# Kernel optimization log

Hardware: AMD Instinct MI355X
Metric: run time of the kernel (lower is better)

The kernel has to match this reference:

```python
import jax, jax.numpy as jnp
import numpy as np

B, T, D, H, DK, DV, FF = 4, 1024, 1024, 16, 64, 64, 4096


def setup_inputs() -> dict:
    key = jax.random.key(0)
    ks = jax.random.split(key, 16)
    sc = 0.02  # init scale (original uses uninitialized torch.empty; use small randn)
    n = lambda k, shape: jax.random.normal(k, shape, jnp.float32) * sc
    return dict(
        x=jax.random.normal(ks[0], (B, T, D), jnp.float32),
        y=jax.random.normal(ks[1], (B, T, D), jnp.float32),
        Wq1=n(ks[2], (H, D, DK)), Wk1=n(ks[3], (H, D, DK)),
        Wv1=n(ks[4], (H, D, DV)), Wo1=n(ks[5], (D, D)),
        Wq2=n(ks[6], (H, D, DK)), Wk2=n(ks[7], (H, D, DK)),
        Wv2=n(ks[8], (H, D, DV)), Wo2=n(ks[9], (D, D)),
        W_in=n(ks[10], (FF, D)), b_in=jnp.zeros((FF,), jnp.float32),
        W_out=n(ks[11], (D, FF)), b_out=jnp.zeros((D,), jnp.float32),
    )


def _mha(q, k, v, Wq, Wk, Wv, Wo):
    # per-head projections: (B,T,D) x (H,D,dk) -> (B,H,T,dk)
    WQ = jnp.einsum('btd,hdk->bhtk', q, Wq)
    WK = jnp.einsum('bsd,hdk->bhsk', k, Wk)
    WV = jnp.einsum('bsd,hdv->bhsv', v, Wv)
    scores = jnp.einsum('bhtk,bhsk->bhts', WQ, WK) / jnp.sqrt(jnp.float32(DK))
    # NOTE: original code softmaxes over dim=2 (the QUERY axis), kept faithfully
    attn = jax.nn.softmax(scores, axis=2)
    partial = jnp.einsum('bhts,bhsv->bhtv', attn, WV)
    partial = partial.transpose(0, 2, 1, 3).reshape(q.shape[0], q.shape[1], -1)  # (B,T,H*dv)
    return partial @ Wo


def _sub_norm(o):
    mean = o.mean(-1, keepdims=True)
    std = o.std(-1, ddof=1, keepdims=True)  # torch.std default is unbiased
    return o - mean - std  # faithful: subtract (not divide by) std


def reference(x, y, Wq1, Wk1, Wv1, Wo1, Wq2, Wk2, Wv2, Wo2, W_in, b_in, W_out, b_out):
    out1 = _sub_norm(_mha(y, y, y, Wq1, Wk1, Wv1, Wo1) + y)
    out2 = _sub_norm(_mha(y, x, x, Wq2, Wk2, Wv2, Wo2) + out1)
    ff = jax.nn.relu(y @ W_in.T + b_in) @ W_out.T + b_out  # FFN applied to y, as in source
    return _sub_norm(ff + out2)
```

## Files before the change

kernel.cpp:

```cpp
#include <hip/hip_runtime.h>


typedef unsigned short u16;
typedef __bf16 bf16x8 __attribute__((ext_vector_type(8)));
typedef float f32x4 __attribute__((ext_vector_type(4)));

__device__ __forceinline__ u16 f2bf(float f) {
    unsigned int u = __float_as_uint(f);
    u += 0x7fffu + ((u >> 16) & 1u);
    return (u16)(u >> 16);
}
__device__ __forceinline__ float bf2f(u16 b) {
    return __uint_as_float(((unsigned int)b) << 16);
}

typedef __attribute__((address_space(1))) const void* as1cv;
typedef __attribute__((address_space(3))) void* as3v;
__device__ __forceinline__ void gl_lds16(const void* g, void* l) {
    __builtin_amdgcn_global_load_lds((as1cv)g, (as3v)l, 16, 0, 0);
}


__global__ __launch_bounds__(256) void convert_f2b_k(const float* __restrict__ in, u16* __restrict__ out) {
    long i = (long)blockIdx.x * 256 + threadIdx.x;
    float4 v = reinterpret_cast<const float4*>(in)[i];
    ushort4 o;
    o.x = f2bf(v.x); o.y = f2bf(v.y); o.z = f2bf(v.z); o.w = f2bf(v.w);
    reinterpret_cast<ushort4*>(out)[i] = o;
}

__global__ __launch_bounds__(256) void pack_perm_t(const float* __restrict__ in, u16* __restrict__ out,
                                                   int Q, int R) {
    __shared__ float tile[64][65];
    int p = blockIdx.z;
    int r0 = blockIdx.x * 64, q0 = blockIdx.y * 64;
    int tx = threadIdx.x & 63, ty = threadIdx.x >> 6;
    const float* inp = in + ((long)p * Q + q0) * R + r0;
    #pragma unroll
    for (int i = 0; i < 64; i += 4)
        tile[ty + i][tx] = inp[(long)(ty + i) * R + tx];
    __syncthreads();
    u16* outp = out + ((long)p * R + r0) * Q + q0;
    #pragma unroll
    for (int i = 0; i < 64; i += 4)
        outp[(long)(ty + i) * Q + tx] = f2bf(tile[tx][ty + i]);
}

__global__ __launch_bounds__(256) void transpose_k(const u16* __restrict__ in, long ld_in, long z_in,
                                                   u16* __restrict__ out, long ld_out, long z_out) {
    __shared__ u16 tile[64][66];
    const u16* inz = in + (long)blockIdx.z * z_in;
    u16* outz = out + (long)blockIdx.z * z_out;
    int r0 = blockIdx.y * 64;
    int c0 = blockIdx.x * 64;
    int tx = threadIdx.x & 63, ty = threadIdx.x >> 6;
    #pragma unroll
    for (int i = 0; i < 64; i += 4)
        tile[ty + i][tx] = inz[(long)(r0 + ty + i) * ld_in + c0 + tx];
    __syncthreads();
    #pragma unroll
    for (int i = 0; i < 64; i += 4)
        outz[(long)(c0 + ty + i) * ld_out + r0 + tx] = tile[tx][ty + i];
}

template<int BM, int BN, int BK, int WM, int WN, int OUT_BF16, int EPI, int SWZ, int KS>
__global__ __launch_bounds__(256) void gemm_k(
    const u16* __restrict__ A, long lda, long a_zin, long a_zout,
    const u16* __restrict__ B, long ldb, long b_zin, long b_zout,
    void* __restrict__ Cv, long ldc, long c_zin, long c_zout,
    int zin, int K, float alpha, const float* __restrict__ bias,
    float* __restrict__ csum)
{
    static_assert(BK == 64, "staging assumes BK=64");
    constexpr int WTM = BM / WM;
    constexpr int WTN = BN / WN;
    constexpr int TM = WTM / 16;
    constexpr int TN = WTN / 16;
    __shared__ __align__(16) u16 smem[(BM + BN) * BK];
    u16* As = smem;
    u16* Bs = smem + BM * BK;

    int bx, by, z;
    if (SWZ == 4) {
        int L = blockIdx.x;
        if (KS > 1) { z = L >> 9; L &= 511; } else { z = 0; }
        by = (L & 7) * 4 + ((L >> 3) & 3);
        bx = L >> 5;
    } else {
        bx = blockIdx.x; by = blockIdx.y; z = blockIdx.z;
    }
    int zi = z % zin, zo = z / zin;
    A += (long)zi * a_zin + (long)zo * a_zout;
    B += (long)zi * b_zin + (long)zo * b_zout;
    long coff = (long)zi * c_zin + (long)zo * c_zout;

    int tid = threadIdx.x;
    int lane = tid & 63;
    int wave = tid >> 6;
    int wm = wave / WN, wn = wave % WN;
    long bm0 = (long)by * BM, bn0 = (long)bx * BN;

    f32x4 acc[TM][TN];
    #pragma unroll
    for (int i = 0; i < TM; ++i)
        #pragma unroll
        for (int j = 0; j < TN; ++j) {
            acc[i][j][0] = 0.f; acc[i][j][1] = 0.f;
            acc[i][j][2] = 0.f; acc[i][j][3] = 0.f;
        }

    int r16 = lane & 15;
    int quad = lane >> 4;
    int l8 = lane >> 3;
    int gsw = ((lane & 7) ^ l8) * 8;

    constexpr int ASTR = BM / 8;
    constexpr int BSTR = BN / 8;

    for (int k0 = 0; k0 < K; k0 += BK) {
        #pragma unroll
        for (int s = wave; s < ASTR; s += 4)
            gl_lds16(&A[(bm0 + s * 8 + l8) * lda + k0 + gsw], &As[s * 512]);
        #pragma unroll
        for (int s = wave; s < BSTR; s += 4)
            gl_lds16(&B[(bn0 + s * 8 + l8) * ldb + k0 + gsw], &Bs[s * 512]);
        __syncthreads();
        #pragma unroll
        for (int kk = 0; kk < BK; kk += 32) {
            int cb = (kk >> 3) + quad;
            bf16x8 av[TM], bv[TN];
            #pragma unroll
            for (int i = 0; i < TM; ++i) {
                int r = wm * WTM + i * 16 + r16;
                av[i] = *reinterpret_cast<const bf16x8*>(&As[r * 64 + ((cb ^ (r & 7)) * 8)]);
            }
            #pragma unroll
            for (int j = 0; j < TN; ++j) {
                int r = wn * WTN + j * 16 + r16;
                bv[j] = *reinterpret_cast<const bf16x8*>(&Bs[r * 64 + ((cb ^ (r & 7)) * 8)]);
            }
            #pragma unroll
            for (int i = 0; i < TM; ++i)
                #pragma unroll
                for (int j = 0; j < TN; ++j)
                    acc[i][j] = __builtin_amdgcn_mfma_f32_16x16x32_bf16(av[i], bv[j], acc[i][j], 0, 0, 0);
        }
        __syncthreads();
    }

    int rb = quad * 4;

    if (EPI == 4) {
        float csl[TN];
        #pragma unroll
        for (int j = 0; j < TN; ++j) csl[j] = 0.f;
        #pragma unroll
        for (int i = 0; i < TM; ++i)
            #pragma unroll
            for (int j = 0; j < TN; ++j)
                #pragma unroll
                for (int r = 0; r < 4; ++r)
                    csl[j] += __expf(acc[i][j][r] * alpha);
        #pragma unroll
        for (int j = 0; j < TN; ++j) {
            float cs = csl[j];
            cs += __shfl_xor(cs, 16, 64);
            cs += __shfl_xor(cs, 32, 64);
            if (quad == 0) {
                long col = bn0 + wn * WTN + j * 16 + r16;
                atomicAdd(&csum[((long)zo * zin + zi) * 1024 + col], cs);
            }
        }
        return;
    }

    constexpr int EB = OUT_BF16 ? 2 : 4;
    constexpr int CH = 16 / EB;
    constexpr int STRIDE = BN + CH;
    constexpr int LDSB = (BM + BN) * BK * 2;
    constexpr int EPASS = (BM * STRIDE * EB > LDSB) ? 2 : 1;
    constexpr int RPP = BM / EPASS;
    static_assert(RPP * STRIDE * EB <= LDSB, "epilogue tile overflows LDS");
    static_assert(EPASS == 1 || (WM == 2 && WTM == RPP), "pass/wave row alignment");
    constexpr int CPR = BN / CH;
    constexpr int NCH = RPP * CPR / 256;
    static_assert(RPP * CPR % 256 == 0, "store mapping");

    float* Ef = reinterpret_cast<float*>(smem);
    char* Cb = reinterpret_cast<char*>(Cv);

    for (int pass = 0; pass < EPASS; ++pass) {
        int p0 = pass * RPP;
        __syncthreads();
        #pragma unroll
        for (int i = 0; i < TM; ++i) {
            #pragma unroll
            for (int j = 0; j < TN; ++j) {
                int lcol = wn * WTN + j * 16 + r16;
                float bsv = (EPI == 1 || EPI == 2) ? bias[bn0 + lcol] : 0.f;
                #pragma unroll
                for (int r = 0; r < 4; ++r) {
                    int lrow = wm * WTM + i * 16 + rb + r;
                    if ((unsigned)(lrow - p0) < (unsigned)RPP) {
                        float v = acc[i][j][r] * alpha;
                        if (EPI == 1) { v += bsv; v = v > 0.f ? v : 0.f; }
                        else if (EPI == 2) { v += bsv; }
                        if (OUT_BF16) smem[(lrow - p0) * STRIDE + lcol] = f2bf(v);
                        else          Ef[(lrow - p0) * STRIDE + lcol] = v;
                    }
                }
            }
        }
        __syncthreads();
        #pragma unroll
        for (int c = 0; c < NCH; ++c) {
            int cid = tid + c * 256;
            int row = cid / CPR, ch = cid - row * CPR;
            int4 v = *reinterpret_cast<const int4*>(
                reinterpret_cast<const char*>(smem) + (row * STRIDE + ch * CH) * EB);
            long gidx = coff + (bm0 + p0 + row) * ldc + bn0 + ch * CH;
            *reinterpret_cast<int4*>(Cb + gidx * EB) = v;
        }
    }
}


__device__ __forceinline__ void bar_raw() {
    asm volatile("" ::: "memory");
    __builtin_amdgcn_s_barrier();
    asm volatile("" ::: "memory");
}

template<int N> __device__ __forceinline__ void vmw() {
    if constexpr (N == 10) asm volatile("s_waitcnt vmcnt(10)" ::: "memory");
    else if constexpr (N == 8) asm volatile("s_waitcnt vmcnt(8)" ::: "memory");
    else if constexpr (N == 4) asm volatile("s_waitcnt vmcnt(4)" ::: "memory");
    else if constexpr (N == 2) asm volatile("s_waitcnt vmcnt(2)" ::: "memory");
    else if constexpr (N == 0) asm volatile("s_waitcnt vmcnt(0)" ::: "memory");
}

__device__ __forceinline__ void stage_half(const u16* __restrict__ base, long ld, int kt,
                                           u16* __restrict__ lds, int half, int wave) {
    const u16* src = base + (long)kt * 64;
    #pragma unroll
    for (int u = 0; u < 2; ++u) {
        int s = half * 16 + u * 8 + wave;
        gl_lds16(src + (long)(s * 8) * ld, lds + s * 512);
    }
}

template<int IH>
__device__ __forceinline__ void read_a8(bf16x8 (&av)[4][2], const u16* __restrict__ As,
                                        int wm, int r16, int quad) {
    #pragma unroll
    for (int ii = 0; ii < 4; ++ii) {
        int r = IH * 128 + wm * 64 + ii * 16 + r16;
        #pragma unroll
        for (int kx = 0; kx < 2; ++kx)
            av[ii][kx] = *reinterpret_cast<const bf16x8*>(&As[r * 64 + (((kx * 4 + quad) ^ (r & 7)) * 8)]);
    }
}

template<int JH>
__device__ __forceinline__ void read_b8(bf16x8 (&bv)[2][2], const u16* __restrict__ Bs,
                                        int wn, int r16, int quad) {
    #pragma unroll
    for (int j = 0; j < 2; ++j) {
        int r = JH * 128 + wn * 32 + j * 16 + r16;
        #pragma unroll
        for (int kx = 0; kx < 2; ++kx)
            bv[j][kx] = *reinterpret_cast<const bf16x8*>(&Bs[r * 64 + (((kx * 4 + quad) ^ (r & 7)) * 8)]);
    }
}

template<int IH, int JH>
__device__ __forceinline__ void mfma_q(f32x4 (&acc)[2][4][2][2],
                                       const bf16x8 (&av)[4][2], const bf16x8 (&bv)[2][2]) {
    #pragma unroll
    for (int kx = 0; kx < 2; ++kx)
        #pragma unroll
        for (int ii = 0; ii < 4; ++ii)
            #pragma unroll
            for (int j = 0; j < 2; ++j)
                acc[IH][ii][JH][j] = __builtin_amdgcn_mfma_f32_16x16x32_bf16(
                    av[ii][kx], bv[j][kx], acc[IH][ii][JH][j], 0, 0, 0);
}

template<int MODE>
__device__ __forceinline__ void tile_iter(
    int t, f32x4 (&acc)[2][4][2][2], bf16x8 (&av)[4][2], bf16x8 (&bvh)[2][2][2],
    u16* __restrict__ smem, const u16* __restrict__ Ab, long lda,
    const u16* __restrict__ Bb, long ldb, int wave, int wm, int wn, int r16, int quad)
{
    u16* As0 = smem + (t & 1) * 32768;
    u16* Bs0 = As0 + 16384;
    u16* As1 = smem + ((t + 1) & 1) * 32768;
    read_a8<0>(av, As0, wm, r16, quad);
    read_b8<0>(bvh[0], Bs0, wn, r16, quad);
    if (MODE < 2) stage_half(Ab, lda, t + 1, As1, 1, wave);
    vmw<MODE == 0 ? 10 : (MODE == 1 ? 10 : 2)>();
    bar_raw();
    __builtin_amdgcn_s_setprio(1);
    mfma_q<0, 0>(acc, av, bvh[0]);
    __builtin_amdgcn_s_setprio(0);
    bar_raw();
    read_b8<1>(bvh[1], Bs0, wn, r16, quad);
    if (MODE == 0) stage_half(Ab, lda, t + 2, As0, 0, wave);
    vmw<MODE == 0 ? 10 : (MODE == 1 ? 8 : 0)>();
    bar_raw();
    __builtin_amdgcn_s_setprio(1);
    mfma_q<0, 1>(acc, av, bvh[1]);
    __builtin_amdgcn_s_setprio(0);
    bar_raw();
    read_a8<1>(av, As0, wm, r16, quad);
    if (MODE == 0) stage_half(Bb, ldb, t + 2, Bs0, 0, wave);
    bar_raw();
    __builtin_amdgcn_s_setprio(1);
    mfma_q<1, 0>(acc, av, bvh[0]);
    __builtin_amdgcn_s_setprio(0);
    bar_raw();
    if (MODE == 0) stage_half(Bb, ldb, t + 2, Bs0, 1, wave);
    if (MODE < 2) vmw<MODE == 0 ? 10 : 4>();
    bar_raw();
    __builtin_amdgcn_s_setprio(1);
    mfma_q<1, 1>(acc, av, bvh[1]);
    __builtin_amdgcn_s_setprio(0);
    bar_raw();
}

template<int NT, int KS, int EPI, int OUT_BF16>
__global__ __launch_bounds__(512, 2) void gemm8_k(
    const u16* __restrict__ A, long lda,
    const u16* __restrict__ B, long ldb,
    void* __restrict__ Cv, void* __restrict__ Cv2, long ldc,
    int K, float alpha, const float* __restrict__ bias, long czs)
{
    __shared__ __align__(16) u16 smem[65536];

    int L = blockIdx.x;
    int z = 0;
    if (KS > 1) { z = L / (16 * NT); L -= z * 16 * NT; }
    int by = (L & 7) * 2 + ((L >> 3) & 1);
    int bx = L >> 4;
    if (KS > 1) { A += (long)z * K; B += (long)z * K; }

    int tid = threadIdx.x;
    int lane = tid & 63, wave = tid >> 6;
    int wm = wave >> 2, wn = wave & 3;
    int r16 = lane & 15, quad = lane >> 4, l8 = lane >> 3;
    int gsw = ((lane & 7) ^ l8) * 8;
    long bm0 = (long)by * 256, bn0 = (long)bx * 256;
    const u16* Ab = A + (bm0 + l8) * lda + gsw;
    const u16* Bb = B + (bn0 + l8) * ldb + gsw;

    f32x4 acc[2][4][2][2];
    #pragma unroll
    for (int a0 = 0; a0 < 2; ++a0)
        #pragma unroll
        for (int a1 = 0; a1 < 4; ++a1)
            #pragma unroll
            for (int a2 = 0; a2 < 2; ++a2)
                #pragma unroll
                for (int a3 = 0; a3 < 2; ++a3) {
                    acc[a0][a1][a2][a3][0] = 0.f; acc[a0][a1][a2][a3][1] = 0.f;
                    acc[a0][a1][a2][a3][2] = 0.f; acc[a0][a1][a2][a3][3] = 0.f;
                }
    bf16x8 av[4][2];
    bf16x8 bvh[2][2][2];

    int T = K >> 6;

    stage_half(Ab, lda, 0, smem,         0, wave);
    stage_half(Bb, ldb, 0, smem + 16384, 0, wave);
    stage_half(Bb, ldb, 0, smem + 16384, 1, wave);
    stage_half(Ab, lda, 0, smem,         1, wave);
    stage_half(Ab, lda, 1, smem + 32768, 0, wave);
    stage_half(Bb, ldb, 1, smem + 49152, 0, wave);
    stage_half(Bb, ldb, 1, smem + 49152, 1, wave);
    vmw<10>();
    bar_raw();

    for (int t = 0; t < T - 2; ++t)
        tile_iter<0>(t, acc, av, bvh, smem, Ab, lda, Bb, ldb, wave, wm, wn, r16, quad);
    tile_iter<1>(T - 2, acc, av, bvh, smem, Ab, lda, Bb, ldb, wave, wm, wn, r16, quad);
    tile_iter<2>(T - 1, acc, av, bvh, smem, Ab, lda, Bb, ldb, wave, wm, wn, r16, quad);

    constexpr int EB = OUT_BF16 ? 2 : 4;
    constexpr int EPASS = OUT_BF16 ? 1 : 2;
    char* Cb = reinterpret_cast<char*>((KS > 1 && z >= 2) ? Cv2 : Cv);
    if (KS > 1) Cb += (long)(z & 1) * czs * EB;
    float bsv[2][2];
    if (EPI == 1) {
        #pragma unroll
        for (int jh = 0; jh < 2; ++jh)
            #pragma unroll
            for (int j = 0; j < 2; ++j)
                bsv[jh][j] = bias[bn0 + jh * 128 + wn * 32 + j * 16 + r16];
    }
    u16* sm16 = smem;
    float* smf = reinterpret_cast<float*>(smem);
    #pragma unroll
    for (int pass = 0; pass < EPASS; ++pass) {
        bar_raw();
        #pragma unroll
        for (int ih = 0; ih < 2; ++ih) {
            if (EPASS == 2 && ih != pass) continue;
            #pragma unroll
            for (int ii = 0; ii < 4; ++ii)
                #pragma unroll
                for (int jh = 0; jh < 2; ++jh)
                    #pragma unroll
                    for (int j = 0; j < 2; ++j)
                        #pragma unroll
                        for (int r = 0; r < 4; ++r) {
                            int lrow = (EPASS == 2 ? 0 : ih * 128) + wm * 64 + ii * 16 + quad * 4 + r;
                            int lcol = jh * 128 + wn * 32 + j * 16 + r16;
                            float v = acc[ih][ii][jh][j][r] * alpha;
                            if (EPI == 1) { v += bsv[jh][j]; v = v > 0.f ? v : 0.f; }
                            int scol = lcol ^ ((lrow & 7) * 8);
                            if (OUT_BF16) sm16[lrow * 256 + scol] = f2bf(v);
                            else          smf[lrow * 256 + scol] = v;
                        }
        }
        bar_raw();
        constexpr int CH = 16 / EB;
        constexpr int CPR = 256 / CH;
        constexpr int NCH = (OUT_BF16 ? 256 : 128) * CPR / 512;
        #pragma unroll
        for (int c = 0; c < NCH; ++c) {
            int cid = tid + c * 512;
            int row = cid / CPR, ch = cid - row * CPR;
            int col = (ch * CH) ^ ((row & 7) * 8);
            int4 v = *reinterpret_cast<const int4*>(
                reinterpret_cast<const char*>(smem) + ((long)row * 256 + col) * EB);
            long grow = bm0 + pass * 128 + row;
            *reinterpret_cast<int4*>(Cb + (grow * ldc + bn0 + ch * CH) * EB) = v;
        }
    }
}

__global__ __launch_bounds__(256) void attn_pv_k(
    const u16* __restrict__ Qg, long ldq, long qbz,
    const u16* __restrict__ Kg, long ldk, long kbz,
    const u16* __restrict__ Vg,
    u16* __restrict__ outg)
{
    __shared__ __align__(16) u16 Qs[128 * 64];
    __shared__ __align__(16) u16 Ks[64 * 64];
    __shared__ __align__(16) u16 Vs[64 * 64];
    __shared__ __align__(16) u16 Es[128 * 64];

    int L = blockIdx.x;
    int h  = (L & 7) * 2 + ((L >> 3) & 1);
    int tb = (L >> 4) & 7;
    int b  = L >> 7;

    const u16* Q  = Qg + (long)b * qbz + h * 64;
    const u16* Kp = Kg + (long)b * kbz + h * 64;
    const u16* Vp = Vg + (long)b * 1048576 + (long)h * 65536;
    u16* outp = outg + (long)b * 1048576 + (long)tb * 131072 + h * 64;

    int tid = threadIdx.x, lane = tid & 63, wave = tid >> 6;
    int wm = wave >> 1, wn = wave & 1;
    int r16 = lane & 15, quad = lane >> 4, l8 = lane >> 3;
    int gsw = ((lane & 7) ^ l8) * 8;
    long t0 = (long)tb * 128;

    #pragma unroll
    for (int s = wave; s < 16; s += 4)
        gl_lds16(&Q[(t0 + s * 8 + l8) * ldq + gsw], &Qs[s * 512]);

    f32x4 acc[4][2];
    #pragma unroll
    for (int i = 0; i < 4; ++i)
        #pragma unroll
        for (int j = 0; j < 2; ++j) {
            acc[i][j][0] = 0.f; acc[i][j][1] = 0.f;
            acc[i][j][2] = 0.f; acc[i][j][3] = 0.f;
        }

    for (int sc = 0; sc < 16; ++sc) {
        #pragma unroll
        for (int s = wave; s < 8; s += 4) {
            gl_lds16(&Kp[(long)(sc * 64 + s * 8 + l8) * ldk + gsw], &Ks[s * 512]);
            gl_lds16(&Vp[(long)(s * 8 + l8) * 1024 + sc * 64 + gsw], &Vs[s * 512]);
        }
        __syncthreads();

        f32x4 e[4][2];
        #pragma unroll
        for (int i = 0; i < 4; ++i)
            #pragma unroll
            for (int j = 0; j < 2; ++j) {
                e[i][j][0] = 0.f; e[i][j][1] = 0.f;
                e[i][j][2] = 0.f; e[i][j][3] = 0.f;
            }
        #pragma unroll
        for (int kk = 0; kk < 64; kk += 32) {
            int cb = (kk >> 3) + quad;
            bf16x8 av[4], bv[2];
            #pragma unroll
            for (int i = 0; i < 4; ++i) {
                int r = wm * 64 + i * 16 + r16;
                av[i] = *reinterpret_cast<const bf16x8*>(&Qs[r * 64 + ((cb ^ (r & 7)) * 8)]);
            }
            #pragma unroll
            for (int j = 0; j < 2; ++j) {
                int r = wn * 32 + j * 16 + r16;
                bv[j] = *reinterpret_cast<const bf16x8*>(&Ks[r * 64 + ((cb ^ (r & 7)) * 8)]);
            }
            #pragma unroll
            for (int i = 0; i < 4; ++i)
                #pragma unroll
                for (int j = 0; j < 2; ++j)
                    e[i][j] = __builtin_amdgcn_mfma_f32_16x16x32_bf16(av[i], bv[j], e[i][j], 0, 0, 0);
        }
        #pragma unroll
        for (int i = 0; i < 4; ++i)
            #pragma unroll
            for (int j = 0; j < 2; ++j) {
                int lcol = wn * 32 + j * 16 + r16;
                #pragma unroll
                for (int r = 0; r < 4; ++r) {
                    int lrow = wm * 64 + i * 16 + quad * 4 + r;
                    float v = __expf(e[i][j][r] * 0.125f);
                    Es[lrow * 64 + (((lcol >> 3) ^ (lrow & 7)) * 8) + (lcol & 7)] = f2bf(v);
                }
            }
        __syncthreads();

        #pragma unroll
        for (int kk = 0; kk < 64; kk += 32) {
            int cb = (kk >> 3) + quad;
            bf16x8 av[4], bv[2];
            #pragma unroll
            for (int i = 0; i < 4; ++i) {
                int r = wm * 64 + i * 16 + r16;
                av[i] = *reinterpret_cast<const bf16x8*>(&Es[r * 64 + ((cb ^ (r & 7)) * 8)]);
            }
            #pragma unroll
            for (int j = 0; j < 2; ++j) {
                int r = wn * 32 + j * 16 + r16;
                bv[j] = *reinterpret_cast<const bf16x8*>(&Vs[r * 64 + ((cb ^ (r & 7)) * 8)]);
            }
            #pragma unroll
            for (int i = 0; i < 4; ++i)
                #pragma unroll
                for (int j = 0; j < 2; ++j)
                    acc[i][j] = __builtin_amdgcn_mfma_f32_16x16x32_bf16(av[i], bv[j], acc[i][j], 0, 0, 0);
        }
        __syncthreads();
    }

    #pragma unroll
    for (int i = 0; i < 4; ++i)
        #pragma unroll
        for (int j = 0; j < 2; ++j) {
            int lcol = wn * 32 + j * 16 + r16;
            #pragma unroll
            for (int r = 0; r < 4; ++r) {
                int lrow = wm * 64 + i * 16 + quad * 4 + r;
                outp[(long)lrow * 1024 + lcol] = f2bf(acc[i][j][r]);
            }
        }
}

__global__ __launch_bounds__(256) void vscale_k(u16* __restrict__ Vt, const float* __restrict__ csum) {
    long idx = (long)blockIdx.x * 256 + threadIdx.x;
    int slab = (int)(idx >> 17);
    int rem = (int)(idx & 131071);
    int hv = rem >> 7;
    int s8 = (rem & 127) * 8;
    const float* cs = csum + slab * 16384 + (hv >> 6) * 1024 + s8;
    u16* pv = Vt + (long)slab * 1048576 + (long)hv * 1024 + s8;
    ushort4 a = *reinterpret_cast<ushort4*>(pv);
    ushort4 b = *reinterpret_cast<ushort4*>(pv + 4);
    a.x = f2bf(bf2f(a.x) / cs[0]); a.y = f2bf(bf2f(a.y) / cs[1]);
    a.z = f2bf(bf2f(a.z) / cs[2]); a.w = f2bf(bf2f(a.w) / cs[3]);
    b.x = f2bf(bf2f(b.x) / cs[4]); b.y = f2bf(bf2f(b.y) / cs[5]);
    b.z = f2bf(bf2f(b.z) / cs[6]); b.w = f2bf(bf2f(b.w) / cs[7]);
    *reinterpret_cast<ushort4*>(pv) = a;
    *reinterpret_cast<ushort4*>(pv + 4) = b;
}

template<int NP, int BIAS>
__global__ __launch_bounds__(256) void addsn_k(const float* __restrict__ parts,
                                               const float* __restrict__ parts2,
                                               long pstride,
                                               const float* __restrict__ resid,
                                               const float* __restrict__ bias,
                                               float* __restrict__ out) {
    __shared__ float sm[8];
    long row = blockIdx.x;
    int tid = threadIdx.x;
    float4 x = reinterpret_cast<const float4*>(resid + row * 1024)[tid];
    #pragma unroll
    for (int p = 0; p < NP; ++p) {
        const float* src = (p < 2) ? (parts + p * pstride) : (parts2 + (p - 2) * pstride);
        float4 a = reinterpret_cast<const float4*>(src + row * 1024)[tid];
        x.x += a.x; x.y += a.y; x.z += a.z; x.w += a.w;
    }
    if (BIAS) {
        float4 bb = reinterpret_cast<const float4*>(bias)[tid];
        x.x += bb.x; x.y += bb.y; x.z += bb.z; x.w += bb.w;
    }
    float s = x.x + x.y + x.z + x.w;
    for (int o = 32; o > 0; o >>= 1) s += __shfl_down(s, o, 64);
    int lane = tid & 63, w = tid >> 6;
    if (lane == 0) sm[w] = s;
    __syncthreads();
    float mean = (sm[0] + sm[1] + sm[2] + sm[3]) * (1.f / 1024.f);
    float d0 = x.x - mean, d1 = x.y - mean, d2 = x.z - mean, d3 = x.w - mean;
    float q = d0 * d0 + d1 * d1 + d2 * d2 + d3 * d3;
    for (int o = 32; o > 0; o >>= 1) q += __shfl_down(q, o, 64);
    if (lane == 0) sm[w + 4] = q;
    __syncthreads();
    float sd = sqrtf((sm[4] + sm[5] + sm[6] + sm[7]) * (1.f / 1023.f));
    float4 ov;
    ov.x = d0 - sd; ov.y = d1 - sd; ov.z = d2 - sd; ov.w = d3 - sd;
    reinterpret_cast<float4*>(out + row * 1024)[tid] = ov;
}


extern "C" void kernel_launch(void* const* d_in, const int* in_sizes, int n_in,
                              void* d_out, int out_size, void* d_ws, size_t ws_size,
                              hipStream_t stream) {
    (void)in_sizes; (void)n_in; (void)out_size; (void)ws_size;
    const float* xf   = (const float*)d_in[0];
    const float* yf   = (const float*)d_in[1];
    const float* Wq1  = (const float*)d_in[2];
    const float* Wk1  = (const float*)d_in[3];
    const float* Wv1  = (const float*)d_in[4];
    const float* Wo1  = (const float*)d_in[5];
    const float* Wq2  = (const float*)d_in[6];
    const float* Wk2  = (const float*)d_in[7];
    const float* Wv2  = (const float*)d_in[8];
    const float* Wo2  = (const float*)d_in[9];
    const float* W_in = (const float*)d_in[10];
    const float* b_in = (const float*)d_in[11];
    const float* W_out= (const float*)d_in[12];
    const float* b_out= (const float*)d_in[13];

    char* p = (char*)d_ws;
    auto alloc = [&](size_t bytes) { char* r = p; p += bytes; return r; };
    u16*   yb    = (u16*)alloc(8388608);
    u16*   xb    = (u16*)alloc(8388608);
    u16*   W1cat = (u16*)alloc(8388608);
    u16*   Wkv2t = (u16*)alloc(4194304);
    u16*   Wo1t  = (u16*)alloc(2097152);
    u16*   Wo2t  = (u16*)alloc(2097152);
    u16*   Winb  = (u16*)alloc(8388608);
    u16*   Woutb = (u16*)alloc(8388608);
    u16*   QKV   = (u16*)alloc(33554432);
    u16*   KV2   = (u16*)alloc(16777216);
    u16*   Vt    = (u16*)alloc(8388608);
    u16*   Pb    = (u16*)alloc(33554432);
    float* csum  = (float*)alloc(262144);
    u16*   part  = (u16*)alloc(8388608);
    float* gout  = (float*)alloc(33554432);
    float* out1  = (float*)alloc(16777216);

    convert_f2b_k<<<4096, 256, 0, stream>>>(yf, yb);
    convert_f2b_k<<<4096, 256, 0, stream>>>(xf, xb);
    pack_perm_t<<<dim3(1, 16, 16), 256, 0, stream>>>(Wq1, W1cat,           1024, 64);
    pack_perm_t<<<dim3(1, 16, 16), 256, 0, stream>>>(Wk1, W1cat + 1048576, 1024, 64);
    pack_perm_t<<<dim3(1, 16, 16), 256, 0, stream>>>(Wv1, W1cat + 2097152, 1024, 64);
    pack_perm_t<<<dim3(1, 16, 16), 256, 0, stream>>>(Wq2, W1cat + 3145728, 1024, 64);
    pack_perm_t<<<dim3(1, 16, 16), 256, 0, stream>>>(Wk2, Wkv2t,           1024, 64);
    pack_perm_t<<<dim3(1, 16, 16), 256, 0, stream>>>(Wv2, Wkv2t + 1048576, 1024, 64);
    pack_perm_t<<<dim3(16, 16, 1), 256, 0, stream>>>(Wo1, Wo1t,            1024, 1024);
    pack_perm_t<<<dim3(16, 16, 1), 256, 0, stream>>>(Wo2, Wo2t,            1024, 1024);
    convert_f2b_k<<<4096, 256, 0, stream>>>(W_in,  Winb);
    convert_f2b_k<<<4096, 256, 0, stream>>>(W_out, Woutb);

    auto run_attention = [&](const u16* Q, long ldq, long qbz,
                             const u16* Kp, long ldk, long kbz,
                             const u16* Vp, long ldv, long vbz) {
        transpose_k<<<dim3(16, 16, 4), 256, 0, stream>>>(Vp, ldv, vbz, Vt, 1024L, 1048576L);
        hipMemsetAsync(csum, 0, 262144, stream);
        gemm_k<128,128,64,2,2,1,4,0,1><<<dim3(8, 8, 64), 256, 0, stream>>>(
            Q, ldq, 64L, qbz, Kp, ldk, 64L, kbz,
            (void*)Pb, 1024L, 0L, 0L, 16, 64, 0.125f, nullptr, csum);
        vscale_k<<<2048, 256, 0, stream>>>(Vt, csum);
        attn_pv_k<<<512, 256, 0, stream>>>(Q, ldq, qbz, Kp, ldk, kbz, Vt, part);
    };

    gemm8_k<16,1,0,1><<<256, 512, 0, stream>>>(
        yb, 1024L, W1cat, 1024L, (void*)QKV, nullptr, 4096L, 1024, 1.0f, nullptr, 0L);
    gemm8_k<8,1,0,1><<<128, 512, 0, stream>>>(
        xb, 1024L, Wkv2t, 1024L, (void*)KV2, nullptr, 2048L, 1024, 1.0f, nullptr, 0L);

    run_attention(QKV, 4096L, 4194304L, QKV + 1024, 4096L, 4194304L, QKV + 2048, 4096L, 4194304L);
    gemm_k<128,64,64,2,2,0,0,4,2><<<dim3(2 * 512), 256, 0, stream>>>(
        part, 1024L, 0L, 512L, Wo1t, 1024L, 0L, 512L,
        (void*)gout, 1024L, 0L, 4194304L, 1, 512, 1.0f, nullptr, nullptr);
    addsn_k<2,0><<<4096, 256, 0, stream>>>(gout, nullptr, 4194304L, yf, nullptr, out1);

    run_attention(QKV + 3072, 4096L, 4194304L, KV2, 2048L, 2097152L, KV2 + 1024, 2048L, 2097152L);
    gemm_k<128,64,64,2,2,0,0,4,2><<<dim3(2 * 512), 256, 0, stream>>>(
        part, 1024L, 0L, 512L, Wo2t, 1024L, 0L, 512L,
        (void*)gout, 1024L, 0L, 4194304L, 1, 512, 1.0f, nullptr, nullptr);
    addsn_k<2,0><<<4096, 256, 0, stream>>>(gout, nullptr, 4194304L, out1, nullptr, (float*)d_out);

    gemm8_k<16,1,1,1><<<256, 512, 0, stream>>>(
        yb, 1024L, Winb, 1024L, (void*)Pb, nullptr, 4096L, 1024, 1.0f, b_in, 0L);
    gemm8_k<4,4,0,0><<<256, 512, 0, stream>>>(
        Pb, 4096L, Woutb, 4096L, (void*)gout, (void*)QKV, 1024L, 1024, 1.0f, nullptr, 4194304L);
    addsn_k<4,1><<<4096, 256, 0, stream>>>(gout, (const float*)QKV, 4194304L,
                                           (const float*)d_out, b_out, (float*)d_out);
}
```

Measured before the change: 516.3 us.

## Software-pipeline LDS fragment reads against MFMA phases in GEMM main loop

```diff
diff --git a/kernel.cpp b/kernel.cpp
--- a/kernel.cpp
+++ b/kernel.cpp
@@ -234,6 +234,7 @@
 template<int N> __device__ __forceinline__ void vmw() {
     if constexpr (N == 10) asm volatile("s_waitcnt vmcnt(10)" ::: "memory");
     else if constexpr (N == 8) asm volatile("s_waitcnt vmcnt(8)" ::: "memory");
+    else if constexpr (N == 6) asm volatile("s_waitcnt vmcnt(6)" ::: "memory");
     else if constexpr (N == 4) asm volatile("s_waitcnt vmcnt(4)" ::: "memory");
     else if constexpr (N == 2) asm volatile("s_waitcnt vmcnt(2)" ::: "memory");
     else if constexpr (N == 0) asm volatile("s_waitcnt vmcnt(0)" ::: "memory");
@@ -288,42 +289,46 @@
 
 template<int MODE>
 __device__ __forceinline__ void tile_iter(
-    int t, f32x4 (&acc)[2][4][2][2], bf16x8 (&av)[4][2], bf16x8 (&bvh)[2][2][2],
+    int t, f32x4 (&acc)[2][4][2][2],
+    bf16x8 (&avP)[4][2], bf16x8 (&avQ)[4][2],
+    bf16x8 (&bvR)[2][2], bf16x8 (&bvS)[2][2],
     u16* __restrict__ smem, const u16* __restrict__ Ab, long lda,
     const u16* __restrict__ Bb, long ldb, int wave, int wm, int wn, int r16, int quad)
 {
     u16* As0 = smem + (t & 1) * 32768;
     u16* Bs0 = As0 + 16384;
     u16* As1 = smem + ((t + 1) & 1) * 32768;
-    read_a8<0>(av, As0, wm, r16, quad);
-    read_b8<0>(bvh[0], Bs0, wn, r16, quad);
+    u16* Bs1 = As1 + 16384;
     if (MODE < 2) stage_half(Ab, lda, t + 1, As1, 1, wave);
     vmw<MODE == 0 ? 10 : (MODE == 1 ? 10 : 2)>();
     bar_raw();
     __builtin_amdgcn_s_setprio(1);
-    mfma_q<0, 0>(acc, av, bvh[0]);
+    read_b8<1>(bvS, Bs0, wn, r16, quad);
+    mfma_q<0, 0>(acc, avP, bvR);
     __builtin_amdgcn_s_setprio(0);
     bar_raw();
-    read_b8<1>(bvh[1], Bs0, wn, r16, quad);
     if (MODE == 0) stage_half(Ab, lda, t + 2, As0, 0, wave);
     vmw<MODE == 0 ? 10 : (MODE == 1 ? 8 : 0)>();
     bar_raw();
     __builtin_amdgcn_s_setprio(1);
-    mfma_q<0, 1>(acc, av, bvh[1]);
+    read_a8<1>(avQ, As0, wm, r16, quad);
+    mfma_q<0, 1>(acc, avP, bvS);
     __builtin_amdgcn_s_setprio(0);
     bar_raw();
-    read_a8<1>(av, As0, wm, r16, quad);
     if (MODE == 0) stage_half(Bb, ldb, t + 2, Bs0, 0, wave);
+    if (MODE == 0) vmw<10>(); else if (MODE == 1) vmw<6>();
     bar_raw();
     __builtin_amdgcn_s_setprio(1);
-    mfma_q<1, 0>(acc, av, bvh[0]);
+    if (MODE < 2) read_a8<0>(avP, As1, wm, r16, quad);
+    mfma_q<1, 0>(acc, avQ, bvR);
     __builtin_amdgcn_s_setprio(0);
     bar_raw();
     if (MODE == 0) stage_half(Bb, ldb, t + 2, Bs0, 1, wave);
-    if (MODE < 2) vmw<MODE == 0 ? 10 : 4>();
+    if (MODE == 0) vmw<10>(); else if (MODE == 1) vmw<4>();
     bar_raw();
     __builtin_amdgcn_s_setprio(1);
-    mfma_q<1, 1>(acc, av, bvh[1]);
+    if (MODE < 2) read_b8<0>(bvR, Bs1, wn, r16, quad);
+    mfma_q<1, 1>(acc, avQ, bvS);
     __builtin_amdgcn_s_setprio(0);
     bar_raw();
 }
@@ -365,8 +370,8 @@
                     acc[a0][a1][a2][a3][0] = 0.f; acc[a0][a1][a2][a3][1] = 0.f;
                     acc[a0][a1][a2][a3][2] = 0.f; acc[a0][a1][a2][a3][3] = 0.f;
                 }
-    bf16x8 av[4][2];
-    bf16x8 bvh[2][2][2];
+    bf16x8 avP[4][2], avQ[4][2];
+    bf16x8 bvR[2][2], bvS[2][2];
 
     int T = K >> 6;
 
@@ -379,11 +384,13 @@
     stage_half(Bb, ldb, 1, smem + 49152, 1, wave);
     vmw<10>();
     bar_raw();
+    read_a8<0>(avP, smem,         wm, r16, quad);
+    read_b8<0>(bvR, smem + 16384, wn, r16, quad);
 
     for (int t = 0; t < T - 2; ++t)
-        tile_iter<0>(t, acc, av, bvh, smem, Ab, lda, Bb, ldb, wave, wm, wn, r16, quad);
-    tile_iter<1>(T - 2, acc, av, bvh, smem, Ab, lda, Bb, ldb, wave, wm, wn, r16, quad);
-    tile_iter<2>(T - 1, acc, av, bvh, smem, Ab, lda, Bb, ldb, wave, wm, wn, r16, quad);
+        tile_iter<0>(t, acc, avP, avQ, bvR, bvS, smem, Ab, lda, Bb, ldb, wave, wm, wn, r16, quad);
+    tile_iter<1>(T - 2, acc, avP, avQ, bvR, bvS, smem, Ab, lda, Bb, ldb, wave, wm, wn, r16, quad);
+    tile_iter<2>(T - 1, acc, avP, avQ, bvR, bvS, smem, Ab, lda, Bb, ldb, wave, wm, wn, r16, quad);
 
     constexpr int EB = OUT_BF16 ? 2 : 4;
     constexpr int EPASS = OUT_BF16 ? 1 : 2;
```

Result: slower. 579.3 us (+12.2%).

## Unroll GEMM main loop by two k-tiles with static LDS buffers and fewer waits

Applied to the files above, without the earlier changes.

```diff
diff --git a/kernel.cpp b/kernel.cpp
--- a/kernel.cpp
+++ b/kernel.cpp
@@ -232,10 +232,7 @@
 }
 
 template<int N> __device__ __forceinline__ void vmw() {
-    if constexpr (N == 10) asm volatile("s_waitcnt vmcnt(10)" ::: "memory");
-    else if constexpr (N == 8) asm volatile("s_waitcnt vmcnt(8)" ::: "memory");
-    else if constexpr (N == 4) asm volatile("s_waitcnt vmcnt(4)" ::: "memory");
-    else if constexpr (N == 2) asm volatile("s_waitcnt vmcnt(2)" ::: "memory");
+    if constexpr (N == 6) asm volatile("s_waitcnt vmcnt(6)" ::: "memory");
     else if constexpr (N == 0) asm volatile("s_waitcnt vmcnt(0)" ::: "memory");
 }
 
@@ -286,44 +283,73 @@
                     av[ii][kx], bv[j][kx], acc[IH][ii][JH][j], 0, 0, 0);
 }
 
-template<int MODE>
-__device__ __forceinline__ void tile_iter(
-    int t, f32x4 (&acc)[2][4][2][2], bf16x8 (&av)[4][2], bf16x8 (&bvh)[2][2][2],
+template<int LAST>
+__device__ __forceinline__ void iter8(
+    int t0, f32x4 (&acc)[2][4][2][2],
+    bf16x8 (&avA)[4][2], bf16x8 (&avB)[4][2],
+    bf16x8 (&bvA)[2][2], bf16x8 (&bvB)[2][2],
     u16* __restrict__ smem, const u16* __restrict__ Ab, long lda,
     const u16* __restrict__ Bb, long ldb, int wave, int wm, int wn, int r16, int quad)
 {
-    u16* As0 = smem + (t & 1) * 32768;
-    u16* Bs0 = As0 + 16384;
-    u16* As1 = smem + ((t + 1) & 1) * 32768;
-    read_a8<0>(av, As0, wm, r16, quad);
-    read_b8<0>(bvh[0], Bs0, wn, r16, quad);
-    if (MODE < 2) stage_half(Ab, lda, t + 1, As1, 1, wave);
-    vmw<MODE == 0 ? 10 : (MODE == 1 ? 10 : 2)>();
+    u16* As0 = smem;
+    u16* Bs0 = smem + 16384;
+    u16* As1 = smem + 32768;
+    u16* Bs1 = smem + 49152;
+    read_a8<0>(avA, As0, wm, r16, quad);
+    read_b8<0>(bvA, Bs0, wn, r16, quad);
+    stage_half(Ab, lda, t0 + 1, As1, 1, wave);
     bar_raw();
     __builtin_amdgcn_s_setprio(1);
-    mfma_q<0, 0>(acc, av, bvh[0]);
+    mfma_q<0, 0>(acc, avA, bvA);
     __builtin_amdgcn_s_setprio(0);
     bar_raw();
-    read_b8<1>(bvh[1], Bs0, wn, r16, quad);
-    if (MODE == 0) stage_half(Ab, lda, t + 2, As0, 0, wave);
-    vmw<MODE == 0 ? 10 : (MODE == 1 ? 8 : 0)>();
+    read_b8<1>(bvB, Bs0, wn, r16, quad);
+    if (!LAST) stage_half(Ab, lda, t0 + 2, As0, 0, wave);
     bar_raw();
     __builtin_amdgcn_s_setprio(1);
-    mfma_q<0, 1>(acc, av, bvh[1]);
+    mfma_q<0, 1>(acc, avA, bvB);
     __builtin_amdgcn_s_setprio(0);
     bar_raw();
-    read_a8<1>(av, As0, wm, r16, quad);
-    if (MODE == 0) stage_half(Bb, ldb, t + 2, Bs0, 0, wave);
+    read_a8<1>(avB, As0, wm, r16, quad);
+    if (!LAST) stage_half(Bb, ldb, t0 + 2, Bs0, 0, wave);
     bar_raw();
     __builtin_amdgcn_s_setprio(1);
-    mfma_q<1, 0>(acc, av, bvh[0]);
+    mfma_q<1, 0>(acc, avB, bvA);
     __builtin_amdgcn_s_setprio(0);
     bar_raw();
-    if (MODE == 0) stage_half(Bb, ldb, t + 2, Bs0, 1, wave);
-    if (MODE < 2) vmw<MODE == 0 ? 10 : 4>();
+    if (!LAST) { stage_half(Bb, ldb, t0 + 2, Bs0, 1, wave); vmw<6>(); }
+    else       { vmw<0>(); }
     bar_raw();
     __builtin_amdgcn_s_setprio(1);
-    mfma_q<1, 1>(acc, av, bvh[1]);
+    mfma_q<1, 1>(acc, avB, bvB);
+    __builtin_amdgcn_s_setprio(0);
+    bar_raw();
+    read_a8<0>(avA, As1, wm, r16, quad);
+    read_b8<0>(bvA, Bs1, wn, r16, quad);
+    if (!LAST) stage_half(Ab, lda, t0 + 2, As0, 1, wave);
+    bar_raw();
+    __builtin_amdgcn_s_setprio(1);
+    mfma_q<0, 0>(acc, avA, bvA);
+    __builtin_amdgcn_s_setprio(0);
+    bar_raw();
+    read_b8<1>(bvB, Bs1, wn, r16, quad);
+    if (!LAST) stage_half(Ab, lda, t0 + 3, As1, 0, wave);
+    bar_raw();
+    __builtin_amdgcn_s_setprio(1);
+    mfma_q<0, 1>(acc, avA, bvB);
+    __builtin_amdgcn_s_setprio(0);
+    bar_raw();
+    read_a8<1>(avB, As1, wm, r16, quad);
+    if (!LAST) stage_half(Bb, ldb, t0 + 3, Bs1, 0, wave);
+    bar_raw();
+    __builtin_amdgcn_s_setprio(1);
+    mfma_q<1, 0>(acc, avB, bvA);
+    __builtin_amdgcn_s_setprio(0);
+    bar_raw();
+    if (!LAST) { stage_half(Bb, ldb, t0 + 3, Bs1, 1, wave); vmw<6>(); }
+    bar_raw();
+    __builtin_amdgcn_s_setprio(1);
+    mfma_q<1, 1>(acc, avB, bvB);
     __builtin_amdgcn_s_setprio(0);
     bar_raw();
 }
@@ -365,8 +391,8 @@
                     acc[a0][a1][a2][a3][0] = 0.f; acc[a0][a1][a2][a3][1] = 0.f;
                     acc[a0][a1][a2][a3][2] = 0.f; acc[a0][a1][a2][a3][3] = 0.f;
                 }
-    bf16x8 av[4][2];
-    bf16x8 bvh[2][2][2];
+    bf16x8 avA[4][2], avB[4][2];
+    bf16x8 bvA[2][2], bvB[2][2];
 
     int T = K >> 6;
 
@@ -377,13 +403,13 @@
     stage_half(Ab, lda, 1, smem + 32768, 0, wave);
     stage_half(Bb, ldb, 1, smem + 49152, 0, wave);
     stage_half(Bb, ldb, 1, smem + 49152, 1, wave);
-    vmw<10>();
-    bar_raw();
-
-    for (int t = 0; t < T - 2; ++t)
-        tile_iter<0>(t, acc, av, bvh, smem, Ab, lda, Bb, ldb, wave, wm, wn, r16, quad);
-    tile_iter<1>(T - 2, acc, av, bvh, smem, Ab, lda, Bb, ldb, wave, wm, wn, r16, quad);
-    tile_iter<2>(T - 1, acc, av, bvh, smem, Ab, lda, Bb, ldb, wave, wm, wn, r16, quad);
+    vmw<6>();
+    bar_raw();
+
+    int ITER = T >> 1;
+    for (int i = 0; i < ITER - 1; ++i)
+        iter8<0>(2 * i, acc, avA, avB, bvA, bvB, smem, Ab, lda, Bb, ldb, wave, wm, wn, r16, quad);
+    iter8<1>(T - 2, acc, avA, avB, bvA, bvB, smem, Ab, lda, Bb, ldb, wave, wm, wn, r16, quad);
 
     constexpr int EB = OUT_BF16 ? 2 : 4;
     constexpr int EPASS = OUT_BF16 ? 1 : 2;
```

Result: slower. 608.1 us (+17.8%).
